# Performance work log

Hardware: AMD Instinct MI355X
Metric: run time of the kernel (lower is better)

Reference implementation:

```python
import jax, jax.numpy as jnp
import numpy as np

TEMPERATURE = 0.07
TOP_MARGIN = 0.95
BOTTOM_MARGIN = 0.05

BATCH = 8192
DIM = 1024


def setup_inputs() -> dict:
    key = jax.random.key(0)
    kA, kB = jax.random.split(key)
    embedding_A = jax.random.normal(kA, (BATCH, DIM), dtype=jnp.float32)
    embedding_B = jax.random.normal(kB, (BATCH, DIM), dtype=jnp.float32)
    return {"embedding_A": embedding_A, "embedding_B": embedding_B}


def _l2norm(x):
    return x * jax.lax.rsqrt(jnp.sum(x * x, axis=-1, keepdims=True))


def reference(embedding_A, embedding_B):
    a = _l2norm(embedding_A)
    b = _l2norm(embedding_B)
    B = a.shape[0]
    sim = a @ b.T                                   # [B, B]
    pos = jnp.diagonal(sim)                         # [B]
    eye = jnp.eye(B, dtype=bool)
    upper = pos[:, None] * TOP_MARGIN
    lower = pos[:, None] * BOTTOM_MARGIN
    neg_mask = (sim <= upper) & (sim >= lower) & ~eye   # [B, B]

    # Per-row CE over [positive, hard negatives] == masked logsumexp - pos/tau.
    z = sim / TEMPERATURE
    full_mask = neg_mask | eye                      # positive always included
    masked = jnp.where(full_mask, z, -jnp.inf)
    m = jnp.max(masked, axis=1, keepdims=True)      # finite: diag always present
    lse = m[:, 0] + jnp.log(jnp.sum(jnp.exp(masked - m), axis=1))
    per_row = lse - pos / TEMPERATURE               # [B]

    valid = jnp.any(neg_mask, axis=1)               # rows with >=1 negative
    count = jnp.sum(valid)
    total = jnp.sum(jnp.where(valid, per_row, 0.0))
    return total / jnp.maximum(count, 1).astype(total.dtype)
```

## Files before the change

kernel.cpp:

```cpp
#include <hip/hip_runtime.h>
#include <hip/hip_bf16.h>

#define BATCH 8192
#define DIM   1024
#define INV_TAU (1.0f / 0.07f)
#define TOPM 0.95f
#define BOTM 0.05f

#define BM 256
#define BN 256
#define BK 64
#define NT (DIM / BK)

typedef __attribute__((ext_vector_type(4))) float f32x4;
typedef __attribute__((ext_vector_type(8))) short bf16x8;

typedef __attribute__((address_space(3))) void       lds_void_t;
typedef const __attribute__((address_space(1))) void gbl_void_t;

__device__ inline void async_copy16(const void* g, void* l) {
    __builtin_amdgcn_global_load_lds((gbl_void_t*)g, (lds_void_t*)l, 16, 0, 0);
}

__device__ inline unsigned short f2bf(float f) {
    __hip_bfloat16 h = __float2bfloat16(f);
    return *reinterpret_cast<unsigned short*>(&h);
}

__global__ __launch_bounds__(256) void prep_kernel(
    const float* __restrict__ A, const float* __restrict__ B,
    unsigned short* __restrict__ An, unsigned short* __restrict__ Bn,
    float* __restrict__ pos, float* __restrict__ S)
{
    int row = blockIdx.x;
    int t = threadIdx.x;
    const float4* a4 = (const float4*)(A + (size_t)row * DIM);
    const float4* b4 = (const float4*)(B + (size_t)row * DIM);
    float4 av = a4[t];
    float4 bv = b4[t];
    float sa = av.x*av.x + av.y*av.y + av.z*av.z + av.w*av.w;
    float sb = bv.x*bv.x + bv.y*bv.y + bv.z*bv.z + bv.w*bv.w;
    float dp = av.x*bv.x + av.y*bv.y + av.z*bv.z + av.w*bv.w;
    #pragma unroll
    for (int d = 32; d > 0; d >>= 1) {
        sa += __shfl_down(sa, d);
        sb += __shfl_down(sb, d);
        dp += __shfl_down(dp, d);
    }
    __shared__ float red[3][4];
    int lane = t & 63, w = t >> 6;
    if (lane == 0) { red[0][w] = sa; red[1][w] = sb; red[2][w] = dp; }
    __syncthreads();
    sa = red[0][0] + red[0][1] + red[0][2] + red[0][3];
    sb = red[1][0] + red[1][1] + red[1][2] + red[1][3];
    dp = red[2][0] + red[2][1] + red[2][2] + red[2][3];
    float ra = rsqrtf(sa);
    float rb = rsqrtf(sb);
    if (t == 0) {
        pos[row] = dp * ra * rb;
        S[row] = 0.0f;
    }
    ushort4 oa, ob;
    oa.x = f2bf(av.x * ra); oa.y = f2bf(av.y * ra);
    oa.z = f2bf(av.z * ra); oa.w = f2bf(av.w * ra);
    ob.x = f2bf(bv.x * rb); ob.y = f2bf(bv.y * rb);
    ob.z = f2bf(bv.z * rb); ob.w = f2bf(bv.w * rb);
    ((ushort4*)(An + (size_t)row * DIM))[t] = oa;
    ((ushort4*)(Bn + (size_t)row * DIM))[t] = ob;
}

__global__ __launch_bounds__(512, 2) void sim_loss_kernel(
    const unsigned short* __restrict__ An, const unsigned short* __restrict__ Bn,
    const float* __restrict__ pos, float* __restrict__ S)
{
    __shared__ char lds[131072];

    int tid  = threadIdx.x;
    int lane = tid & 63;
    int wave = tid >> 6;
    int wm = wave >> 2, wn = wave & 3;
    int fr = lane & 15;
    int q  = lane >> 4;

    int bid = blockIdx.x;

#define BASES(g, rB, cB) do {                                                        \
    int xcd_ = bid & 7, jj_ = bid >> 3;                                              \
    int qr_ = (g) >> 1, qc_ = ((g) & 1) ^ (qr_ & 1);                                 \
    (rB) = (qr_ * 16 + (xcd_ >> 1) * 4 + (jj_ >> 3)) * BM;                           \
    (cB) = (qc_ * 16 + (xcd_ & 1) * 8 + (jj_ & 7)) * BN;                             \
} while (0)

    f32x4 acc[8][4] = {};
    bf16x8 a[4][2];
    bf16x8 b0[2][2];
    bf16x8 b1[2][2];

    int sw = (fr & 7) << 4;
    int c0 = (q * 16) ^ sw;
    int c1 = (64 + q * 16) ^ sw;
    int aRow = (wm * 128 + fr) * 128;
    int bRow = (wn * 64 + fr) * 128;

    int strow = tid >> 3;
    int scb   = ((tid & 7) * 16) ^ ((strow & 7) << 4);
    int ldst = tid * 16;

#define PANELS(rB, cB, pA, pB) do {                                                  \
    (pA) = (const char*)An + (size_t)((rB) + strow) * 2048 + scb;                    \
    (pB) = (const char*)Bn + (size_t)((cB) + strow) * 2048 + scb;                    \
} while (0)

#define STAGE(gbase, u, h, ldsdst) do {                                              \
    async_copy16((gbase) + (size_t)(h) * 262144 + (size_t)(u) * 128,                 \
                 (ldsdst) + (h) * 16384 + ldst);                                     \
    async_copy16((gbase) + (size_t)(h) * 262144 + 131072 + (size_t)(u) * 128,        \
                 (ldsdst) + (h) * 16384 + 8192 + ldst);                              \
} while (0)

#define LDA_(p, mh) do {                                                             \
    const char* _s = lds + (p) * 32768;                                              \
    _Pragma("unroll") for (int m = 0; m < 4; ++m) {                                  \
        a[m][0] = *(const bf16x8*)(_s + aRow + (mh) * 8192 + m * 2048 + c0);         \
        a[m][1] = *(const bf16x8*)(_s + aRow + (mh) * 8192 + m * 2048 + c1);         \
    }                                                                                \
} while (0)

#define LDB_(arr, p, nh) do {                                                        \
    const char* _s = lds + 65536 + (p) * 32768;                                      \
    _Pragma("unroll") for (int n = 0; n < 2; ++n) {                                  \
        arr[n][0] = *(const bf16x8*)(_s + bRow + (nh) * 4096 + n * 2048 + c0);       \
        arr[n][1] = *(const bf16x8*)(_s + bRow + (nh) * 4096 + n * 2048 + c1);       \
    }                                                                                \
} while (0)

#define MM_(barr, mo, no) do {                                                       \
    _Pragma("unroll") for (int m = 0; m < 4; ++m)                                    \
    _Pragma("unroll") for (int n = 0; n < 2; ++n) {                                  \
        acc[(mo)+m][(no)+n] = __builtin_amdgcn_mfma_f32_16x16x32_bf16(               \
            a[m][0], barr[n][0], acc[(mo)+m][(no)+n], 0, 0, 0);                      \
        acc[(mo)+m][(no)+n] = __builtin_amdgcn_mfma_f32_16x16x32_bf16(               \
            a[m][1], barr[n][1], acc[(mo)+m][(no)+n], 0, 0, 0);                      \
    }                                                                                \
} while (0)

#define BAR() __builtin_amdgcn_s_barrier()
#define SCH() __builtin_amdgcn_sched_barrier(0)
#define LGKM0() asm volatile("s_waitcnt lgkmcnt(0)" ::: "memory")
#define VMC(n)  asm volatile("s_waitcnt vmcnt(" #n ")" ::: "memory")
#define PRI1() __builtin_amdgcn_s_setprio(1)
#define PRI0() __builtin_amdgcn_s_setprio(0)

#define KTILE(p, pA_, uA, pB_, uB) do {                                              \
    char* stA = lds + ((p) ^ 1) * 32768;                                             \
    char* stB = lds + 65536 + (p) * 32768;                                           \
                                                 \
    BAR(); SCH();                                                                    \
    LDA_((p), 0); LDB_(b0, (p), 0); LDB_(b1, (p), 1);                                \
    STAGE((pA_), (uA), 0, stA); STAGE((pA_), (uA), 1, stA);                          \
    PRI1(); MM_(b0, 0, 0); MM_(b1, 0, 2); PRI0();                                    \
    LGKM0();                                                                         \
                                                 \
    BAR(); SCH();                                                                    \
    LDA_((p), 1);                                                                    \
    STAGE((pB_), (uB), 0, stB); STAGE((pB_), (uB), 1, stB);                          \
    PRI1(); MM_(b1, 4, 2); MM_(b0, 4, 0); PRI0();                                    \
    LGKM0(); VMC(4);                                                                 \
} while (0)

    int rowB, colB;
    BASES(0, rowB, colB);
    const char *gAc, *gBc;
    PANELS(rowB, colB, gAc, gBc);

    STAGE(gAc, 0, 0, lds);
    STAGE(gAc, 0, 1, lds);
    STAGE(gBc, 0, 0, lds + 65536);
    STAGE(gBc, 0, 1, lds + 65536);
    STAGE(gBc, 1, 0, lds + 98304);
    STAGE(gBc, 1, 1, lds + 98304);
    VMC(4);

    #pragma unroll 1
    for (int g = 0; g < 4; ++g) {
        int gn = (g < 3) ? g + 1 : 3;
        int rowBn, colBn;
        BASES(gn, rowBn, colBn);
        const char *gAn2, *gBn2;
        PANELS(rowBn, colBn, gAn2, gBn2);

        #pragma unroll 1
        for (int tt = 0; tt < 7; ++tt) {
            KTILE(0, gAc, 2 * tt + 1, gBc, 2 * tt + 2);
            KTILE(1, gAc, 2 * tt + 2, gBc, 2 * tt + 3);
        }
        KTILE(0, gAc, 15, gBn2, 0);
        KTILE(1, gAn2, 0, gBn2, 1);

        #pragma unroll
        for (int m = 0; m < 8; ++m) {
            #pragma unroll
            for (int j2 = 0; j2 < 4; ++j2) {
                int i = rowB + wm * 128 + m * 16 + q * 4 + j2;
                float p  = pos[i];
                float up = TOPM * p, lo = BOTM * p;
                float rs = 0.0f;
                #pragma unroll
                for (int n = 0; n < 4; ++n) {
                    float sv = acc[m][n][j2];
                    int col = colB + wn * 64 + n * 16 + fr;
                    if (sv <= up && sv >= lo && col != i)
                        rs += __expf((sv - p) * INV_TAU);
                }
                #pragma unroll
                for (int d = 1; d < 16; d <<= 1)
                    rs += __shfl_xor(rs, d);
                if (fr == 0 && rs != 0.0f)
                    atomicAdd(&S[i], rs);
            }
        }
        #pragma unroll
        for (int m2 = 0; m2 < 8; ++m2)
            #pragma unroll
            for (int n2 = 0; n2 < 4; ++n2)
                acc[m2][n2] = (f32x4){0.0f, 0.0f, 0.0f, 0.0f};

        gAc = gAn2; gBc = gBn2; rowB = rowBn; colB = colBn;
    }
    LGKM0();
    VMC(0);

#undef BASES
#undef PANELS
#undef STAGE
#undef LDA_
#undef LDB_
#undef MM_
#undef BAR
#undef SCH
#undef LGKM0
#undef VMC
#undef PRI1
#undef PRI0
#undef KTILE
}

__global__ __launch_bounds__(256) void finalize_kernel(
    const float* __restrict__ S, float* __restrict__ out)
{
    int t = threadIdx.x;
    float tot = 0.0f;
    int c = 0;
    for (int i = t; i < BATCH; i += 256) {
        float s = S[i];
        if (s > 0.0f) { tot += log1pf(s); c += 1; }
    }
    #pragma unroll
    for (int d = 32; d > 0; d >>= 1) {
        tot += __shfl_down(tot, d);
        c   += __shfl_down(c, d);
    }
    __shared__ float st[4];
    __shared__ int   sc[4];
    int lane = t & 63, w = t >> 6;
    if (lane == 0) { st[w] = tot; sc[w] = c; }
    __syncthreads();
    if (t == 0) {
        float T = st[0] + st[1] + st[2] + st[3];
        int   C = sc[0] + sc[1] + sc[2] + sc[3];
        out[0] = T / (float)(C > 0 ? C : 1);
    }
}

extern "C" void kernel_launch(void* const* d_in, const int* in_sizes, int n_in,
                              void* d_out, int out_size, void* d_ws, size_t ws_size,
                              hipStream_t stream) {
    const float* A = (const float*)d_in[0];
    const float* B = (const float*)d_in[1];

    char* ws = (char*)d_ws;
    unsigned short* An = (unsigned short*)ws;
    unsigned short* Bn = An + (size_t)BATCH * DIM;
    float* pos = (float*)(Bn + (size_t)BATCH * DIM);
    float* S   = pos + BATCH;
    float* out = (float*)d_out;

    prep_kernel<<<BATCH, 256, 0, stream>>>(A, B, An, Bn, pos, S);
    sim_loss_kernel<<<256, 512, 0, stream>>>(An, Bn, pos, S);
    finalize_kernel<<<1, 256, 0, stream>>>(S, out);
}
```

Measured before the change: 201.7 us.

## Load A fragments directly from global into registers, halve LDS to B only

The A operand is no longer staged through LDS. Each wave loads its own A fragments straight from global memory into registers, double-buffered across k-steps, while only the B panel keeps the async global-to-LDS path, so LDS shrinks from 128KB to 64KB. This removes the LDS write and read traffic for A and frees LDS capacity. In exchange, waves that share A rows each fetch them from global/L2 separately, which adds global traffic and exposes load latency, managed by vmcnt waits.

```diff
diff --git a/kernel.cpp b/kernel.cpp
--- a/kernel.cpp
+++ b/kernel.cpp
@@ -73,7 +73,7 @@
     const unsigned short* __restrict__ An, const unsigned short* __restrict__ Bn,
     const float* __restrict__ pos, float* __restrict__ S)
 {
-    __shared__ char lds[131072];
+    __shared__ char lds[65536];
 
     int tid  = threadIdx.x;
     int lane = tid & 63;
@@ -92,23 +92,25 @@
 } while (0)
 
     f32x4 acc[8][4] = {};
-    bf16x8 a[4][2];
+    bf16x8 a0[4][2];
+    bf16x8 a1[4][2];
     bf16x8 b0[2][2];
     bf16x8 b1[2][2];
 
     int sw = (fr & 7) << 4;
     int c0 = (q * 16) ^ sw;
     int c1 = (64 + q * 16) ^ sw;
-    int aRow = (wm * 128 + fr) * 128;
     int bRow = (wn * 64 + fr) * 128;
 
     int strow = tid >> 3;
     int scb   = ((tid & 7) * 16) ^ ((strow & 7) << 4);
     int ldst = tid * 16;
 
-#define PANELS(rB, cB, pA, pB) do {                                                  \
-    (pA) = (const char*)An + (size_t)((rB) + strow) * 2048 + scb;                    \
+#define BPANEL(cB, pB) do {                                                          \
     (pB) = (const char*)Bn + (size_t)((cB) + strow) * 2048 + scb;                    \
+} while (0)
+#define APANEL(rB, pA) do {                                                          \
+    (pA) = (const char*)An + (size_t)((rB) + wm * 128 + fr) * 2048 + q * 16;         \
 } while (0)
 
 #define STAGE(gbase, u, h, ldsdst) do {                                              \
@@ -118,29 +120,28 @@
                  (ldsdst) + (h) * 16384 + 8192 + ldst);                              \
 } while (0)
 
-#define LDA_(p, mh) do {                                                             \
+#define GLA(arr, base, mhrows) do {                                                  \
+    _Pragma("unroll") for (int m = 0; m < 4; ++m) {                                  \
+        arr[m][0] = *(const bf16x8*)((base) + (size_t)((mhrows) + m * 16) * 2048);   \
+        arr[m][1] = *(const bf16x8*)((base) + (size_t)((mhrows) + m * 16) * 2048 + 64);\
+    }                                                                                \
+} while (0)
+
+#define LDB_(arr, p, nh) do {                                                        \
     const char* _s = lds + (p) * 32768;                                              \
-    _Pragma("unroll") for (int m = 0; m < 4; ++m) {                                  \
-        a[m][0] = *(const bf16x8*)(_s + aRow + (mh) * 8192 + m * 2048 + c0);         \
-        a[m][1] = *(const bf16x8*)(_s + aRow + (mh) * 8192 + m * 2048 + c1);         \
-    }                                                                                \
-} while (0)
-
-#define LDB_(arr, p, nh) do {                                                        \
-    const char* _s = lds + 65536 + (p) * 32768;                                      \
     _Pragma("unroll") for (int n = 0; n < 2; ++n) {                                  \
         arr[n][0] = *(const bf16x8*)(_s + bRow + (nh) * 4096 + n * 2048 + c0);       \
         arr[n][1] = *(const bf16x8*)(_s + bRow + (nh) * 4096 + n * 2048 + c1);       \
     }                                                                                \
 } while (0)
 
-#define MM_(barr, mo, no) do {                                                       \
+#define MMA_(aarr, barr, mo, no) do {                                                \
     _Pragma("unroll") for (int m = 0; m < 4; ++m)                                    \
     _Pragma("unroll") for (int n = 0; n < 2; ++n) {                                  \
         acc[(mo)+m][(no)+n] = __builtin_amdgcn_mfma_f32_16x16x32_bf16(               \
-            a[m][0], barr[n][0], acc[(mo)+m][(no)+n], 0, 0, 0);                      \
+            aarr[m][0], barr[n][0], acc[(mo)+m][(no)+n], 0, 0, 0);                   \
         acc[(mo)+m][(no)+n] = __builtin_amdgcn_mfma_f32_16x16x32_bf16(               \
-            a[m][1], barr[n][1], acc[(mo)+m][(no)+n], 0, 0, 0);                      \
+            aarr[m][1], barr[n][1], acc[(mo)+m][(no)+n], 0, 0, 0);                   \
     }                                                                                \
 } while (0)
 
@@ -151,51 +152,54 @@
 #define PRI1() __builtin_amdgcn_s_setprio(1)
 #define PRI0() __builtin_amdgcn_s_setprio(0)
 
-#define KTILE(p, pA_, uA, pB_, uB) do {                                              \
-    char* stA = lds + ((p) ^ 1) * 32768;                                             \
-    char* stB = lds + 65536 + (p) * 32768;                                           \
+#define KTILE(p, pA1, pA0, pB_, uB) do {                                             \
+    char* stB = lds + (p) * 32768;                                                   \
                                                  \
     BAR(); SCH();                                                                    \
-    LDA_((p), 0); LDB_(b0, (p), 0); LDB_(b1, (p), 1);                                \
-    STAGE((pA_), (uA), 0, stA); STAGE((pA_), (uA), 1, stA);                          \
-    PRI1(); MM_(b0, 0, 0); MM_(b1, 0, 2); PRI0();                                    \
+    LDB_(b0, (p), 0); LDB_(b1, (p), 1);                                              \
+    GLA(a1, (pA1), 64);                                                              \
+    VMC(12);                                                                         \
+    PRI1(); MMA_(a0, b0, 0, 0); MMA_(a0, b1, 0, 2); PRI0();                          \
     LGKM0();                                                                         \
                                                  \
     BAR(); SCH();                                                                    \
-    LDA_((p), 1);                                                                    \
+    GLA(a0, (pA0), 0);                                                               \
+    SCH();                                                                           \
     STAGE((pB_), (uB), 0, stB); STAGE((pB_), (uB), 1, stB);                          \
-    PRI1(); MM_(b1, 4, 2); MM_(b0, 4, 0); PRI0();                                    \
-    LGKM0(); VMC(4);                                                                 \
+    VMC(12);                                                                         \
+    PRI1(); MMA_(a1, b1, 4, 2); MMA_(a1, b0, 4, 0); PRI0();                          \
 } while (0)
 
     int rowB, colB;
     BASES(0, rowB, colB);
-    const char *gAc, *gBc;
-    PANELS(rowB, colB, gAc, gBc);
-
-    STAGE(gAc, 0, 0, lds);
-    STAGE(gAc, 0, 1, lds);
-    STAGE(gBc, 0, 0, lds + 65536);
-    STAGE(gBc, 0, 1, lds + 65536);
-    STAGE(gBc, 1, 0, lds + 98304);
-    STAGE(gBc, 1, 1, lds + 98304);
-    VMC(4);
+    const char *gAf, *gBc;
+    APANEL(rowB, gAf);
+    BPANEL(colB, gBc);
+
+    STAGE(gBc, 0, 0, lds);
+    STAGE(gBc, 0, 1, lds);
+    STAGE(gBc, 1, 0, lds + 32768);
+    STAGE(gBc, 1, 1, lds + 32768);
+    GLA(a0, gAf, 0);
+    VMC(0);
+    BAR();
 
     #pragma unroll 1
     for (int g = 0; g < 4; ++g) {
         int gn = (g < 3) ? g + 1 : 3;
         int rowBn, colBn;
         BASES(gn, rowBn, colBn);
-        const char *gAn2, *gBn2;
-        PANELS(rowBn, colBn, gAn2, gBn2);
+        const char *gAfn, *gBn2;
+        APANEL(rowBn, gAfn);
+        BPANEL(colBn, gBn2);
 
         #pragma unroll 1
         for (int tt = 0; tt < 7; ++tt) {
-            KTILE(0, gAc, 2 * tt + 1, gBc, 2 * tt + 2);
-            KTILE(1, gAc, 2 * tt + 2, gBc, 2 * tt + 3);
+            KTILE(0, gAf + (2 * tt) * 128,     gAf + (2 * tt + 1) * 128, gBc, 2 * tt + 2);
+            KTILE(1, gAf + (2 * tt + 1) * 128, gAf + (2 * tt + 2) * 128, gBc, 2 * tt + 3);
         }
-        KTILE(0, gAc, 15, gBn2, 0);
-        KTILE(1, gAn2, 0, gBn2, 1);
+        KTILE(0, gAf + 14 * 128, gAf + 15 * 128, gBn2, 0);
+        KTILE(1, gAf + 15 * 128, gAfn, gBn2, 1);
 
         #pragma unroll
         for (int m = 0; m < 8; ++m) {
@@ -225,17 +229,18 @@
             for (int n2 = 0; n2 < 4; ++n2)
                 acc[m2][n2] = (f32x4){0.0f, 0.0f, 0.0f, 0.0f};
 
-        gAc = gAn2; gBc = gBn2; rowB = rowBn; colB = colBn;
+        gAf = gAfn; gBc = gBn2; rowB = rowBn; colB = colBn;
     }
     LGKM0();
     VMC(0);
 
 #undef BASES
-#undef PANELS
+#undef BPANEL
+#undef APANEL
 #undef STAGE
-#undef LDA_
+#undef GLA
 #undef LDB_
-#undef MM_
+#undef MMA_
 #undef BAR
 #undef SCH
 #undef LGKM0
```

Measured after the change: 408.9 us. 103% more time.

## Restructure K-tile pipeline into three barrier phases with split A register sets

Applied to the files above, without the earlier changes.

Changes the software pipeline of the GEMM main loop. A is now double-buffered the same way as B: both operands for the next k-tile are prefetched two tiles ahead, with the A staging offset aligned to B. Each K-tile now has three barrier-separated phases, and A fragments live in two register sets (a0/a1) so MFMA work can begin after partial LDS reads. All global-to-LDS staging is pushed to the last phase, after both LDS halves have been read. The aim is to overlap LDS reads with MFMA more finely and to remove the lgkm wait before the final phase. The cost is an extra barrier per tile, more VGPRs, and a changed vmcnt wait depth that must still match the prefetch distance.

```diff
diff --git a/kernel.cpp b/kernel.cpp
--- a/kernel.cpp
+++ b/kernel.cpp
@@ -92,7 +92,8 @@
 } while (0)
 
     f32x4 acc[8][4] = {};
-    bf16x8 a[4][2];
+    bf16x8 a0[4][2];
+    bf16x8 a1[4][2];
     bf16x8 b0[2][2];
     bf16x8 b1[2][2];
 
@@ -118,11 +119,11 @@
                  (ldsdst) + (h) * 16384 + 8192 + ldst);                              \
 } while (0)
 
-#define LDA_(p, mh) do {                                                             \
+#define LDA_(arr, p, mh) do {                                                        \
     const char* _s = lds + (p) * 32768;                                              \
     _Pragma("unroll") for (int m = 0; m < 4; ++m) {                                  \
-        a[m][0] = *(const bf16x8*)(_s + aRow + (mh) * 8192 + m * 2048 + c0);         \
-        a[m][1] = *(const bf16x8*)(_s + aRow + (mh) * 8192 + m * 2048 + c1);         \
+        arr[m][0] = *(const bf16x8*)(_s + aRow + (mh) * 8192 + m * 2048 + c0);       \
+        arr[m][1] = *(const bf16x8*)(_s + aRow + (mh) * 8192 + m * 2048 + c1);       \
     }                                                                                \
 } while (0)
 
@@ -134,13 +135,13 @@
     }                                                                                \
 } while (0)
 
-#define MM_(barr, mo, no) do {                                                       \
+#define MMA_(aarr, barr, mo, no) do {                                                \
     _Pragma("unroll") for (int m = 0; m < 4; ++m)                                    \
     _Pragma("unroll") for (int n = 0; n < 2; ++n) {                                  \
         acc[(mo)+m][(no)+n] = __builtin_amdgcn_mfma_f32_16x16x32_bf16(               \
-            a[m][0], barr[n][0], acc[(mo)+m][(no)+n], 0, 0, 0);                      \
+            aarr[m][0], barr[n][0], acc[(mo)+m][(no)+n], 0, 0, 0);                   \
         acc[(mo)+m][(no)+n] = __builtin_amdgcn_mfma_f32_16x16x32_bf16(               \
-            a[m][1], barr[n][1], acc[(mo)+m][(no)+n], 0, 0, 0);                      \
+            aarr[m][1], barr[n][1], acc[(mo)+m][(no)+n], 0, 0, 0);                   \
     }                                                                                \
 } while (0)
 
@@ -152,20 +153,21 @@
 #define PRI0() __builtin_amdgcn_s_setprio(0)
 
 #define KTILE(p, pA_, uA, pB_, uB) do {                                              \
-    char* stA = lds + ((p) ^ 1) * 32768;                                             \
+    char* stA = lds + (p) * 32768;                                                   \
     char* stB = lds + 65536 + (p) * 32768;                                           \
-                                                 \
-    BAR(); SCH();                                                                    \
-    LDA_((p), 0); LDB_(b0, (p), 0); LDB_(b1, (p), 1);                                \
+     BAR(); SCH();                                                           \
+    LDA_(a0, (p), 0); LDB_(b0, (p), 0);                                              \
+    PRI1(); MMA_(a0, b0, 0, 0); PRI0();                                              \
+    LGKM0();                                                                         \
+     BAR(); SCH();                                                           \
+    LDA_(a1, (p), 1); LDB_(b1, (p), 1);                                              \
+    PRI1(); MMA_(a0, b1, 0, 2); PRI0();                                              \
+    LGKM0();                                                                         \
+     BAR(); SCH();                                                           \
     STAGE((pA_), (uA), 0, stA); STAGE((pA_), (uA), 1, stA);                          \
-    PRI1(); MM_(b0, 0, 0); MM_(b1, 0, 2); PRI0();                                    \
-    LGKM0();                                                                         \
-                                                 \
-    BAR(); SCH();                                                                    \
-    LDA_((p), 1);                                                                    \
     STAGE((pB_), (uB), 0, stB); STAGE((pB_), (uB), 1, stB);                          \
-    PRI1(); MM_(b1, 4, 2); MM_(b0, 4, 0); PRI0();                                    \
-    LGKM0(); VMC(4);                                                                 \
+    PRI1(); MMA_(a1, b1, 4, 2); MMA_(a1, b0, 4, 0); PRI0();                          \
+    VMC(8);                                                                          \
 } while (0)
 
     int rowB, colB;
@@ -177,9 +179,11 @@
     STAGE(gAc, 0, 1, lds);
     STAGE(gBc, 0, 0, lds + 65536);
     STAGE(gBc, 0, 1, lds + 65536);
+    STAGE(gAc, 1, 0, lds + 32768);
+    STAGE(gAc, 1, 1, lds + 32768);
     STAGE(gBc, 1, 0, lds + 98304);
     STAGE(gBc, 1, 1, lds + 98304);
-    VMC(4);
+    VMC(0);
 
     #pragma unroll 1
     for (int g = 0; g < 4; ++g) {
@@ -191,11 +195,11 @@
 
         #pragma unroll 1
         for (int tt = 0; tt < 7; ++tt) {
-            KTILE(0, gAc, 2 * tt + 1, gBc, 2 * tt + 2);
-            KTILE(1, gAc, 2 * tt + 2, gBc, 2 * tt + 3);
+            KTILE(0, gAc, 2 * tt + 2, gBc, 2 * tt + 2);
+            KTILE(1, gAc, 2 * tt + 3, gBc, 2 * tt + 3);
         }
-        KTILE(0, gAc, 15, gBn2, 0);
-        KTILE(1, gAn2, 0, gBn2, 1);
+        KTILE(0, gAn2, 0, gBn2, 0);
+        KTILE(1, gAn2, 1, gBn2, 1);
 
         #pragma unroll
         for (int m = 0; m < 8; ++m) {
@@ -235,7 +239,7 @@
 #undef STAGE
 #undef LDA_
 #undef LDB_
-#undef MM_
+#undef MMA_
 #undef BAR
 #undef SCH
 #undef LGKM0
```

Measured after the change: 224.4 us. 1.11x slower.
